# Kernel optimization log

Hardware: AMD Instinct MI355X
Metric: run time of the kernel (lower is better)

Reference implementation:

```python
import jax, jax.numpy as jnp
import numpy as np

B, N, D, L = 32, 1000, 256, 3


def setup_inputs() -> dict:
    key = jax.random.key(0)
    k1, k2, k3, k4 = jax.random.split(key, 4)
    x = jax.random.normal(k1, (B, N, D), dtype=jnp.float32)
    node_feature = jax.random.normal(k2, (B, N, D), dtype=jnp.float32)
    # GCNConv weights (PyG Linear, glorot) and biases, stacked over layers
    scale = jnp.sqrt(6.0 / (D + D)).astype(jnp.float32)
    Ws = jax.random.uniform(k3, (L, D, D), minval=-1.0, maxval=1.0, dtype=jnp.float32) * scale
    bs = jnp.zeros((L, D), dtype=jnp.float32)
    return {"x": x, "node_feature": node_feature, "Ws": Ws, "bs": bs}


def _gcn_norm_adj(n):
    # self_loop=False -> adjacency is all-ones (diagonal included), so
    # add_remaining_self_loops is a no-op; deg = n for every node.
    adj = jnp.ones((n, n), dtype=jnp.float32)
    deg = adj.sum(axis=1)
    dinv = jax.lax.rsqrt(deg)
    return dinv[:, None] * adj * dinv[None, :]  # == ones/n


def reference(x, node_feature, Ws, bs):
    # x is unused by the math (only its size is inspected in the original).
    A_norm = _gcn_norm_adj(node_feature.shape[1])
    h = node_feature
    for l in range(L):
        h = jnp.einsum('bnd,de->bne', h, Ws[l])          # linear transform
        h = jnp.einsum('mn,bnd->bmd', A_norm, h) + bs[l]  # normalized aggregation + bias
        if l < L - 1:
            h = jax.nn.relu(h)  # dropout is identity in eval mode
    update_node_feature = h + node_feature  # residual (unconditional in source)
    return (update_node_feature, node_feature)
```

## Files before the change

### kernel.cpp

```cpp
#include <hip/hip_runtime.h>

#define BB 32
#define NN 1000
#define DD 256
#define SS 25
#define RPS 40
#define ELEMS (BB * NN * DD)

__global__ __launch_bounds__(256) void k_zero(float* __restrict__ p) {
    p[blockIdx.x * 256 + threadIdx.x] = 0.f;
}

__global__ __launch_bounds__(256) void k_colsum(const float* __restrict__ nf,
                                                float* __restrict__ sums) {
    const int s = blockIdx.x, b = blockIdx.y, t = threadIdx.x;
    const int rg = t >> 6, dg = t & 63;
    const float4* src = (const float4*)nf;
    float4 acc = make_float4(0.f, 0.f, 0.f, 0.f);
#pragma unroll
    for (int c = 0; c < RPS / 4; c++) {
        const int n = s * RPS + c * 4 + rg;
        float4 v = src[(b * NN + n) * (DD / 4) + dg];
        acc.x += v.x; acc.y += v.y; acc.z += v.z; acc.w += v.w;
    }
    __shared__ float red[1024];
    ((float4*)red)[rg * 64 + dg] = acc;
    __syncthreads();
    float sum = 0.f;
#pragma unroll
    for (int r = 0; r < 4; r++) sum += red[r * 256 + t];
    atomicAdd(&sums[b * DD + t], sum);
}

__global__ __launch_bounds__(256) void k_layer(const float* __restrict__ Hin,
                                               const float* __restrict__ W,
                                               const float* __restrict__ bias,
                                               float* __restrict__ Hout,
                                               float scale, int relu) {
    const int ds = blockIdx.x, b = blockIdx.y, t = threadIdx.x;
    const int kg = t >> 5, dl = t & 31;
    const int d = ds * 32 + dl;
    __shared__ float h[DD];
    __shared__ float red[256];
    h[t] = Hin[b * DD + t] * scale;
    __syncthreads();
    float acc = 0.f;
#pragma unroll
    for (int kk = 0; kk < 32; kk++) {
        const int k = kg * 32 + kk;
        acc += h[k] * W[k * DD + d];
    }
    red[t] = acc;
    __syncthreads();
    if (kg == 0) {
        float o = acc;
#pragma unroll
        for (int r = 1; r < 8; r++) o += red[r * 32 + dl];
        o += bias[d];
        if (relu) o = fmaxf(o, 0.f);
        Hout[b * DD + d] = o;
    }
}

__global__ __launch_bounds__(256) void k_out(const float* __restrict__ nf,
                                             const float* __restrict__ hrow,
                                             float* __restrict__ out) {
    const int i = blockIdx.x * 256 + threadIdx.x;
    const int e = i * 4;
    const int b = e / (NN * DD);
    const int d0 = e & (DD - 1);
    float4 v = ((const float4*)nf)[i];
    float4 hv = *(const float4*)(hrow + b * DD + d0);
    float4 o = make_float4(v.x + hv.x, v.y + hv.y, v.z + hv.z, v.w + hv.w);
    ((float4*)out)[i] = o;
    ((float4*)(out + ELEMS))[i] = v;
}

extern "C" void kernel_launch(void* const* d_in, const int* in_sizes, int n_in,
                              void* d_out, int out_size, void* d_ws, size_t ws_size,
                              hipStream_t stream) {
    const float* nf  = (const float*)d_in[1];
    const float* Ws  = (const float*)d_in[2];
    const float* bsv = (const float*)d_in[3];
    float* out = (float*)d_out;

    float* sums = (float*)d_ws;
    float* hA   = sums + BB * DD;
    float* hB   = hA   + BB * DD;

    k_zero<<<BB * DD / 256, 256, 0, stream>>>(sums);
    k_colsum<<<dim3(SS, BB), 256, 0, stream>>>(nf, sums);
    k_layer<<<dim3(8, BB), 256, 0, stream>>>(sums, Ws + 0 * DD * DD, bsv + 0 * DD,
                                             hA, 1.0f / (float)NN, 1);
    k_layer<<<dim3(8, BB), 256, 0, stream>>>(hA, Ws + 1 * DD * DD, bsv + 1 * DD,
                                             hB, 1.0f, 1);
    k_layer<<<dim3(8, BB), 256, 0, stream>>>(hB, Ws + 2 * DD * DD, bsv + 2 * DD,
                                             hA, 1.0f, 0);
    k_out<<<(ELEMS / 4) / 256, 256, 0, stream>>>(nf, hA, out);
}
```

Before: 127.1 us.

## Fuse passthrough copy into colsum, merge three layers into one MLP kernel

New measurement: 150.1 us. 1.18x slower.

```diff
diff --git a/kernel.cpp b/kernel.cpp
--- a/kernel.cpp
+++ b/kernel.cpp
@@ -3,77 +3,81 @@
 #define BB 32
 #define NN 1000
 #define DD 256
-#define SS 25
-#define RPS 40
+#define SS 50
+#define RPS 20
 #define ELEMS (BB * NN * DD)
 
-__global__ __launch_bounds__(256) void k_zero(float* __restrict__ p) {
-    p[blockIdx.x * 256 + threadIdx.x] = 0.f;
-}
-
-__global__ __launch_bounds__(256) void k_colsum(const float* __restrict__ nf,
-                                                float* __restrict__ sums) {
+__global__ __launch_bounds__(256) void k_colsum_copy(const float4* __restrict__ nf4,
+                                                     float4* __restrict__ out1_4,
+                                                     float* __restrict__ partials) {
     const int s = blockIdx.x, b = blockIdx.y, t = threadIdx.x;
-    const int rg = t >> 6, dg = t & 63;
-    const float4* src = (const float4*)nf;
+    const int r4 = t >> 6, c = t & 63;
     float4 acc = make_float4(0.f, 0.f, 0.f, 0.f);
 #pragma unroll
-    for (int c = 0; c < RPS / 4; c++) {
-        const int n = s * RPS + c * 4 + rg;
-        float4 v = src[(b * NN + n) * (DD / 4) + dg];
+    for (int i = 0; i < RPS / 4; i++) {
+        const int n = s * RPS + i * 4 + r4;
+        const int idx = (b * NN + n) * (DD / 4) + c;
+        float4 v = nf4[idx];
+        out1_4[idx] = v;
         acc.x += v.x; acc.y += v.y; acc.z += v.z; acc.w += v.w;
     }
     __shared__ float red[1024];
-    ((float4*)red)[rg * 64 + dg] = acc;
+    ((float4*)red)[r4 * 64 + c] = acc;
     __syncthreads();
-    float sum = 0.f;
-#pragma unroll
-    for (int r = 0; r < 4; r++) sum += red[r * 256 + t];
-    atomicAdd(&sums[b * DD + t], sum);
+    const float sum = red[t] + red[256 + t] + red[512 + t] + red[768 + t];
+    partials[(b * SS + s) * DD + t] = sum;
 }
 
-__global__ __launch_bounds__(256) void k_layer(const float* __restrict__ Hin,
-                                               const float* __restrict__ W,
-                                               const float* __restrict__ bias,
-                                               float* __restrict__ Hout,
-                                               float scale, int relu) {
-    const int ds = blockIdx.x, b = blockIdx.y, t = threadIdx.x;
-    const int kg = t >> 5, dl = t & 31;
-    const int d = ds * 32 + dl;
+__global__ __launch_bounds__(1024) void k_mlp(const float* __restrict__ partials,
+                                              const float* __restrict__ Ws,
+                                              const float* __restrict__ bsv,
+                                              float* __restrict__ hrow) {
+    const int b = blockIdx.x, t = threadIdx.x;
+    const int d = t & (DD - 1), kq = t >> 8;
     __shared__ float h[DD];
-    __shared__ float red[256];
-    h[t] = Hin[b * DD + t] * scale;
-    __syncthreads();
+    __shared__ float red[1024];
+
     float acc = 0.f;
-#pragma unroll
-    for (int kk = 0; kk < 32; kk++) {
-        const int k = kg * 32 + kk;
-        acc += h[k] * W[k * DD + d];
-    }
+    for (int s = kq; s < SS; s += 4)
+        acc += partials[(b * SS + s) * DD + d];
     red[t] = acc;
     __syncthreads();
-    if (kg == 0) {
-        float o = acc;
-#pragma unroll
-        for (int r = 1; r < 8; r++) o += red[r * 32 + dl];
-        o += bias[d];
-        if (relu) o = fmaxf(o, 0.f);
-        Hout[b * DD + d] = o;
+    if (kq == 0)
+        h[d] = (red[d] + red[DD + d] + red[2 * DD + d] + red[3 * DD + d]) * (1.0f / (float)NN);
+    __syncthreads();
+
+    for (int l = 0; l < 3; l++) {
+        const float* __restrict__ W = Ws + l * DD * DD;
+        float a = 0.f;
+#pragma unroll 16
+        for (int kk = 0; kk < 64; kk++) {
+            const int k = kq * 64 + kk;
+            a += h[k] * W[k * DD + d];
+        }
+        __syncthreads();
+        red[t] = a;
+        __syncthreads();
+        if (kq == 0) {
+            float o = red[d] + red[DD + d] + red[2 * DD + d] + red[3 * DD + d]
+                      + bsv[l * DD + d];
+            if (l < 2) o = fmaxf(o, 0.f);
+            if (l == 2) hrow[b * DD + d] = o;
+            else        h[d] = o;
+        }
+        __syncthreads();
     }
 }
 
-__global__ __launch_bounds__(256) void k_out(const float* __restrict__ nf,
-                                             const float* __restrict__ hrow,
-                                             float* __restrict__ out) {
+__global__ __launch_bounds__(256) void k_out0(const float4* __restrict__ nf4,
+                                              const float* __restrict__ hrow,
+                                              float4* __restrict__ out0_4) {
     const int i = blockIdx.x * 256 + threadIdx.x;
     const int e = i * 4;
     const int b = e / (NN * DD);
     const int d0 = e & (DD - 1);
-    float4 v = ((const float4*)nf)[i];
+    float4 v = nf4[i];
     float4 hv = *(const float4*)(hrow + b * DD + d0);
-    float4 o = make_float4(v.x + hv.x, v.y + hv.y, v.z + hv.z, v.w + hv.w);
-    ((float4*)out)[i] = o;
-    ((float4*)(out + ELEMS))[i] = v;
+    out0_4[i] = make_float4(v.x + hv.x, v.y + hv.y, v.z + hv.z, v.w + hv.w);
 }
 
 extern "C" void kernel_launch(void* const* d_in, const int* in_sizes, int n_in,
@@ -84,17 +88,11 @@
     const float* bsv = (const float*)d_in[3];
     float* out = (float*)d_out;
 
-    float* sums = (float*)d_ws;
-    float* hA   = sums + BB * DD;
-    float* hB   = hA   + BB * DD;
+    float* partials = (float*)d_ws;
+    float* hrow     = partials + BB * SS * DD;
 
-    k_zero<<<BB * DD / 256, 256, 0, stream>>>(sums);
-    k_colsum<<<dim3(SS, BB), 256, 0, stream>>>(nf, sums);
-    k_layer<<<dim3(8, BB), 256, 0, stream>>>(sums, Ws + 0 * DD * DD, bsv + 0 * DD,
-                                             hA, 1.0f / (float)NN, 1);
-    k_layer<<<dim3(8, BB), 256, 0, stream>>>(hA, Ws + 1 * DD * DD, bsv + 1 * DD,
-                                             hB, 1.0f, 1);
-    k_layer<<<dim3(8, BB), 256, 0, stream>>>(hB, Ws + 2 * DD * DD, bsv + 2 * DD,
-                                             hA, 1.0f, 0);
-    k_out<<<(ELEMS / 4) / 256, 256, 0, stream>>>(nf, hA, out);
+    k_colsum_copy<<<dim3(SS, BB), 256, 0, stream>>>((const float4*)nf,
+                                                    (float4*)(out + ELEMS), partials);
+    k_mlp<<<BB, 1024, 0, stream>>>(partials, Ws, bsv, hrow);
+    k_out0<<<(ELEMS / 4) / 256, 256, 0, stream>>>((const float4*)nf, hrow, (float4*)out);
 }
```
